# Kernel optimization log

Measured on AMD Instinct MI355X. Metric: run time of the kernel, lower is better.

Reference implementation:

```python
import jax, jax.numpy as jnp
import numpy as np


def setup_inputs() -> dict:
    key = jax.random.key(0)
    k1, k2 = jax.random.split(key)
    center = jax.random.normal(k1, (4096,), dtype=jnp.float32)
    error = jax.random.normal(k2, (8192, 4096), dtype=jnp.float32) * 0.01
    return {"center": center, "error": error}


def reference(center, error):
    # Zonotope ReLU abstract transformer.
    center_orig_shape = center.shape
    error_orig_shape = error.shape
    c = center.reshape(-1)                      # (d,)
    e = error.reshape(error.shape[0], -1)       # (n_error, d)
    n_error, d = e.shape

    apt = jnp.sum(jnp.abs(e), axis=0)           # (d,) interval radius
    ub = c + apt
    lb = c - apt

    cross = (ub > 0) & (lb < 0)                 # unstable neurons
    act = lb >= 0                               # stably active
    # dead (ub <= 0): slope = 0, mu = 0 -> center/error zeroed

    denom = jnp.where(cross, ub - lb, jnp.float32(1.0))
    slope = jnp.where(cross, ub / denom, jnp.float32(0.0))
    mu = jnp.where(cross, -slope * lb * jnp.float32(0.5), jnp.float32(0.0))

    new_center = jnp.where(act, c, slope * c + mu)          # (d,)
    col_scale = jnp.where(act, jnp.float32(1.0), slope)     # (d,)
    top = e * col_scale[None, :]                             # (n_error, d)
    # One fresh error term per crossing neuron; padded to d rows (diagonal),
    # zero rows where the neuron is not crossing (static output shape).
    bottom = jnp.diag(mu)                                    # (d, d)
    new_error = jnp.concatenate([top, bottom], axis=0)       # (n_error + d, d)

    new_center = new_center.reshape(center_orig_shape)
    new_error = new_error.reshape((n_error + d,) + error_orig_shape[1:])
    return new_center, new_error
```

## Files before the change

kernel.cpp:

```cpp
#include <hip/hip_runtime.h>

#define D      4096
#define NERR   8192
#define DF4    (D / 4)
#define HROWS  (NERR / 2)
#define TPB    1024
#define RPP    (TPB / 8)
#define NPASS  (HROWS / RPP)
#define NWAVE  (TPB / 64)
#define NBLK   256

typedef float f32x4 __attribute__((ext_vector_type(4)));

__global__ __launch_bounds__(TPB) void k_fused(const f32x4* __restrict__ e4,
                                               const f32x4* __restrict__ c4,
                                               f32x4* __restrict__ oc4,
                                               f32x4* __restrict__ top4,
                                               f32x4* __restrict__ bot4,
                                               float* __restrict__ partf,
                                               int*   __restrict__ bar) {
    __shared__ f32x4 wred[NWAVE * 8];
    __shared__ float aptL[32];
    __shared__ f32x4 scl[8];
    __shared__ f32x4 muL[8];

    const int t    = threadIdx.x;
    const int lane = t & 63;
    const int w    = t >> 6;
    const int cf   = t & 7;
    const int r0   = t >> 3;
    const int s    = blockIdx.x >> 1;
    const int h    = blockIdx.x & 1;
    const int off  = s * 8 + cf;
    const size_t rbase = (size_t)h * HROWS;

    f32x4 acc = (f32x4)(0.f, 0.f, 0.f, 0.f);
    #pragma unroll 8
    for (int k = 0; k < NPASS; ++k) {
        f32x4 v = e4[(rbase + k * RPP + r0) * DF4 + off];
        acc.x += fabsf(v.x);
        acc.y += fabsf(v.y);
        acc.z += fabsf(v.z);
        acc.w += fabsf(v.w);
    }
    #pragma unroll
    for (int st = 8; st <= 32; st <<= 1) {
        acc.x += __shfl_xor(acc.x, st, 64);
        acc.y += __shfl_xor(acc.y, st, 64);
        acc.z += __shfl_xor(acc.z, st, 64);
        acc.w += __shfl_xor(acc.w, st, 64);
    }
    if (lane < 8) wred[w * 8 + lane] = acc;
    __syncthreads();

    if (t < 32) {
        const int f4 = t >> 2, cm = t & 3;
        float sum = 0.f;
        #pragma unroll
        for (int w2 = 0; w2 < NWAVE; ++w2) sum += wred[w2 * 8 + f4][cm];
        __hip_atomic_store(&partf[(2 * s + h) * 32 + t], sum,
                           __ATOMIC_RELAXED, __HIP_MEMORY_SCOPE_AGENT);
    }
    __syncthreads();

    if (t == 0) {
        __threadfence();
        __hip_atomic_fetch_add(&bar[s], 1, __ATOMIC_RELEASE,
                               __HIP_MEMORY_SCOPE_AGENT);
        while (__hip_atomic_load(&bar[s], __ATOMIC_ACQUIRE,
                                 __HIP_MEMORY_SCOPE_AGENT) < 2) {}
    }
    __syncthreads();

    if (t < 32)
        aptL[t] = __hip_atomic_load(&partf[(2 * s) * 32 + t],
                                    __ATOMIC_RELAXED, __HIP_MEMORY_SCOPE_AGENT)
                + __hip_atomic_load(&partf[(2 * s + 1) * 32 + t],
                                    __ATOMIC_RELAXED, __HIP_MEMORY_SCOPE_AGENT);
    __syncthreads();

    if (t < 8) {
        const int g = s * 8 + t;
        const f32x4 cen = c4[g];
        f32x4 oc, cs, mu4;
        #pragma unroll
        for (int j = 0; j < 4; ++j) {
            const float apt = aptL[t * 4 + j];
            const float c  = cen[j];
            const float ub = c + apt;
            const float lb = c - apt;
            const bool cross = (ub > 0.f) && (lb < 0.f);
            const bool act   = (lb >= 0.f);
            const float denom = cross ? (ub - lb) : 1.f;
            const float slope = cross ? (ub / denom) : 0.f;
            const float mu    = cross ? (-slope * lb * 0.5f) : 0.f;
            oc[j]  = act ? c : (slope * c + mu);
            cs[j]  = act ? 1.f : slope;
            mu4[j] = mu;
        }
        scl[t] = cs;
        muL[t] = mu4;
        if (h == 0) oc4[g] = oc;
    }
    __syncthreads();

    const f32x4 cs = scl[cf];
    #pragma unroll 8
    for (int k = 0; k < NPASS; ++k) {
        const size_t idx = (rbase + k * RPP + r0) * DF4 + off;
        f32x4 v = e4[idx];
        v *= cs;
        __builtin_nontemporal_store(v, &top4[idx]);
    }

    const int r  = 32 * s + 16 * h + w;
    const int dg = r >> 2;
    const float muv = muL[(r >> 2) - 8 * s][r & 3];
    #pragma unroll
    for (int j = 0; j < 16; ++j) {
        const int c = lane + j * 64;
        f32x4 v = (f32x4)(0.f, 0.f, 0.f, 0.f);
        if (c == dg) v[r & 3] = muv;
        __builtin_nontemporal_store(v, &bot4[(size_t)r * DF4 + c]);
    }
}

extern "C" void kernel_launch(void* const* d_in, const int* in_sizes, int n_in,
                              void* d_out, int out_size, void* d_ws, size_t ws_size,
                              hipStream_t stream) {
    const float* center = (const float*)d_in[0];
    const float* error  = (const float*)d_in[1];
    float* out = (float*)d_out;
    float* ws  = (float*)d_ws;

    float* partf = ws;
    int*   bar   = (int*)(ws + 256 * 32);

    float* out_center = out;
    float* out_top    = out + D;
    float* out_bottom = out + (size_t)D + (size_t)NERR * D;

    hipMemsetAsync(bar, 0, 128 * sizeof(int), stream);

    k_fused<<<NBLK, TPB, 0, stream>>>(
        (const f32x4*)error, (const f32x4*)center,
        (f32x4*)out_center, (f32x4*)out_top, (f32x4*)out_bottom,
        partf, bar);
}
```

Before: 88.59 us.

## Cache most error tile in registers and LDS to avoid re-reading from HBM

Halves threads per block to 512 and keeps 40 of each thread's 64 loaded error vectors in registers and 7 more in shared memory. The second pass can then scale and store them without reloading from global memory, and only the remaining rows are re-read. The per-pair barrier becomes a single grid-wide counter barrier, and the diagonal bottom writes are interleaved before the final reloads. This trades heavy register and LDS pressure, and a global barrier that needs all 256 blocks co-resident, for less HBM read traffic.

```diff
diff --git a/kernel.cpp b/kernel.cpp
--- a/kernel.cpp
+++ b/kernel.cpp
@@ -4,22 +4,24 @@
 #define NERR   8192
 #define DF4    (D / 4)
 #define HROWS  (NERR / 2)
-#define TPB    1024
-#define RPP    (TPB / 8)
-#define NPASS  (HROWS / RPP)
-#define NWAVE  (TPB / 64)
+#define TPB    512
 #define NBLK   256
+#define NK     64
+#define NREG   40
+#define NLDS   7
+#define NSTAGE (NREG + NLDS)
 
 typedef float f32x4 __attribute__((ext_vector_type(4)));
 
-__global__ __launch_bounds__(TPB) void k_fused(const f32x4* __restrict__ e4,
-                                               const f32x4* __restrict__ c4,
-                                               f32x4* __restrict__ oc4,
-                                               f32x4* __restrict__ top4,
-                                               f32x4* __restrict__ bot4,
-                                               float* __restrict__ partf,
-                                               int*   __restrict__ bar) {
-    __shared__ f32x4 wred[NWAVE * 8];
+__global__ __launch_bounds__(TPB, 2) void k_fused(const f32x4* __restrict__ e4,
+                                                  const f32x4* __restrict__ c4,
+                                                  f32x4* __restrict__ oc4,
+                                                  f32x4* __restrict__ top4,
+                                                  f32x4* __restrict__ bot4,
+                                                  float* __restrict__ partf,
+                                                  int*   __restrict__ bar) {
+    __shared__ f32x4 stage[NLDS * TPB];
+    __shared__ f32x4 wred[8 * 8];
     __shared__ float aptL[32];
     __shared__ f32x4 scl[8];
     __shared__ f32x4 muL[8];
@@ -34,14 +36,17 @@
     const int off  = s * 8 + cf;
     const size_t rbase = (size_t)h * HROWS;
 
+    f32x4 reg[NREG];
     f32x4 acc = (f32x4)(0.f, 0.f, 0.f, 0.f);
-    #pragma unroll 8
-    for (int k = 0; k < NPASS; ++k) {
-        f32x4 v = e4[(rbase + k * RPP + r0) * DF4 + off];
+    #pragma unroll
+    for (int k = 0; k < NK; ++k) {
+        f32x4 v = e4[(rbase + (size_t)k * 64 + r0) * DF4 + off];
         acc.x += fabsf(v.x);
         acc.y += fabsf(v.y);
         acc.z += fabsf(v.z);
         acc.w += fabsf(v.w);
+        if (k < NREG)         reg[k] = v;
+        else if (k < NSTAGE)  stage[(k - NREG) * TPB + t] = v;
     }
     #pragma unroll
     for (int st = 8; st <= 32; st <<= 1) {
@@ -57,25 +62,24 @@
         const int f4 = t >> 2, cm = t & 3;
         float sum = 0.f;
         #pragma unroll
-        for (int w2 = 0; w2 < NWAVE; ++w2) sum += wred[w2 * 8 + f4][cm];
-        __hip_atomic_store(&partf[(2 * s + h) * 32 + t], sum,
+        for (int w2 = 0; w2 < 8; ++w2) sum += wred[w2 * 8 + f4][cm];
+        __hip_atomic_store(&partf[(size_t)blockIdx.x * 32 + t], sum,
                            __ATOMIC_RELAXED, __HIP_MEMORY_SCOPE_AGENT);
     }
     __syncthreads();
 
     if (t == 0) {
-        __threadfence();
-        __hip_atomic_fetch_add(&bar[s], 1, __ATOMIC_RELEASE,
+        __hip_atomic_fetch_add(&bar[0], 1, __ATOMIC_ACQ_REL,
                                __HIP_MEMORY_SCOPE_AGENT);
-        while (__hip_atomic_load(&bar[s], __ATOMIC_ACQUIRE,
-                                 __HIP_MEMORY_SCOPE_AGENT) < 2) {}
+        while (__hip_atomic_load(&bar[0], __ATOMIC_ACQUIRE,
+                                 __HIP_MEMORY_SCOPE_AGENT) < NBLK) {}
     }
     __syncthreads();
 
     if (t < 32)
-        aptL[t] = __hip_atomic_load(&partf[(2 * s) * 32 + t],
+        aptL[t] = __hip_atomic_load(&partf[(size_t)(2 * s) * 32 + t],
                                     __ATOMIC_RELAXED, __HIP_MEMORY_SCOPE_AGENT)
-                + __hip_atomic_load(&partf[(2 * s + 1) * 32 + t],
+                + __hip_atomic_load(&partf[(size_t)(2 * s + 1) * 32 + t],
                                     __ATOMIC_RELAXED, __HIP_MEMORY_SCOPE_AGENT);
     __syncthreads();
 
@@ -105,23 +109,37 @@
     __syncthreads();
 
     const f32x4 cs = scl[cf];
-    #pragma unroll 8
-    for (int k = 0; k < NPASS; ++k) {
-        const size_t idx = (rbase + k * RPP + r0) * DF4 + off;
-        f32x4 v = e4[idx];
-        v *= cs;
+
+    #pragma unroll
+    for (int k = 0; k < NREG; ++k) {
+        f32x4 v = reg[k] * cs;
+        __builtin_nontemporal_store(
+            v, &top4[(rbase + (size_t)k * 64 + r0) * DF4 + off]);
+    }
+    #pragma unroll
+    for (int k = NREG; k < NSTAGE; ++k) {
+        f32x4 v = stage[(k - NREG) * TPB + t] * cs;
+        __builtin_nontemporal_store(
+            v, &top4[(rbase + (size_t)k * 64 + r0) * DF4 + off]);
+    }
+    {
+        const int r   = 32 * s + 16 * h + (t >> 5);
+        const int dg  = r >> 2;
+        const float muv = muL[(r >> 2) - 8 * s][r & 3];
+        const int c0  = t & 31;
+        #pragma unroll
+        for (int j = 0; j < 32; ++j) {
+            const int c = c0 + j * 32;
+            f32x4 v = (f32x4)(0.f, 0.f, 0.f, 0.f);
+            if (c == dg) v[r & 3] = muv;
+            __builtin_nontemporal_store(v, &bot4[(size_t)r * DF4 + c]);
+        }
+    }
+    #pragma unroll
+    for (int k = NSTAGE; k < NK; ++k) {
+        const size_t idx = (rbase + (size_t)k * 64 + r0) * DF4 + off;
+        f32x4 v = e4[idx] * cs;
         __builtin_nontemporal_store(v, &top4[idx]);
-    }
-
-    const int r  = 32 * s + 16 * h + w;
-    const int dg = r >> 2;
-    const float muv = muL[(r >> 2) - 8 * s][r & 3];
-    #pragma unroll
-    for (int j = 0; j < 16; ++j) {
-        const int c = lane + j * 64;
-        f32x4 v = (f32x4)(0.f, 0.f, 0.f, 0.f);
-        if (c == dg) v[r & 3] = muv;
-        __builtin_nontemporal_store(v, &bot4[(size_t)r * DF4 + c]);
     }
 }
 
@@ -134,13 +152,13 @@
     float* ws  = (float*)d_ws;
 
     float* partf = ws;
-    int*   bar   = (int*)(ws + 256 * 32);
+    int*   bar   = (int*)(ws + NBLK * 32);
 
     float* out_center = out;
     float* out_top    = out + D;
     float* out_bottom = out + (size_t)D + (size_t)NERR * D;
 
-    hipMemsetAsync(bar, 0, 128 * sizeof(int), stream);
+    hipMemsetAsync(bar, 0, sizeof(int), stream);
 
     k_fused<<<NBLK, TPB, 0, stream>>>(
         (const f32x4*)error, (const f32x4*)center,
```

After: 87.69 us. No clear change (-1.0%).
